# Kernel tuning notes

Hardware: AMD Instinct MI355X
Metric: run time of the kernel (lower is better)

Reference implementation:

```python
import jax, jax.numpy as jnp
import numpy as np

# DREAMPlace IDXST_IDCT (a.k.a. idsct2): y[u,v] = sum_p sum_q x[p,q] * sin(pi*p*(u+0.5)/M) * cos(pi*q*(v+0.5)/N)
# i.e. IDXST (inverse discrete sine transform, DST-III-like, unnormalized) along the M axis
# and IDCT (DCT-III-like, unnormalized, full weight on k=0) along the N axis.
# Computed with the classic 2N-padded FFT trick using the precomputed twiddles
# expk[k] = exp(-1j*pi*k/(2N)) stored as [N,2] (real, imag), matching precompute_expk.

def _idxt_spectrum(x, expk):
    """F[u] = sum_k x[k] * exp(-1j*pi*k*(2u+1)/(2N)), along last axis.
    Re(F) is the IDCT sum (cos), -Im(F) is the IDXST sum (sin)."""
    N = x.shape[-1]
    c = (x * expk[..., 0]) + 1j * (x * expk[..., 1])  # x[k] * exp(-j*pi*k/(2N))
    z = jnp.concatenate([c, jnp.zeros_like(c)], axis=-1)  # zero-pad to 2N
    return jnp.fft.fft(z, axis=-1)[..., :N]


def idct_1d(x, expk):
    # y[u] = sum_k x[k] cos(pi*k*(2u+1)/(2N))
    return _idxt_spectrum(x, expk).real


def idxst_1d(x, expk):
    # y[u] = sum_k x[k] sin(pi*k*(2u+1)/(2N))
    return -_idxt_spectrum(x, expk).imag


def _make_expk(L):
    k = jnp.arange(L, dtype=jnp.float32) * (np.pi / (2.0 * L))
    return jnp.stack([jnp.cos(k), -jnp.sin(k)], axis=-1)  # exp(-j*pi*k/(2L))


def setup_inputs() -> dict:
    M, N = 4096, 4096
    key = jax.random.key(0)
    x = jax.random.normal(key, (M, N), dtype=jnp.float32)
    return {"x": x, "expkM": _make_expk(M), "expkN": _make_expk(N)}


def reference(x, expkM, expkN):
    # IDCT along the last dim (N), then IDXST along the second-to-last dim (M):
    # idxst(idct(x)^T)^T
    t = idct_1d(x, expkN)                                        # [M, N]
    y = idxst_1d(t.swapaxes(-2, -1), expkM).swapaxes(-2, -1)     # [M, N]
    return y
```

## Files before the change

kernel.cpp:

```cpp
#include <hip/hip_runtime.h>
#include <hip/hip_bf16.h>
#include <stdint.h>
#include <cmath>


typedef __attribute__((ext_vector_type(4))) float f32x4;
typedef __attribute__((ext_vector_type(8))) unsigned short u16x8;
typedef __attribute__((ext_vector_type(8))) __bf16 bf16x8;

__device__ __forceinline__ unsigned short f2bf(float f) {
  union { float f; unsigned u; } v; v.f = f;
  unsigned u = v.u + 0x7fffu + ((v.u >> 16) & 1u);
  return (unsigned short)(u >> 16);
}
__device__ __forceinline__ float bf2f(unsigned short h) {
  union { unsigned u; float f; } v; v.u = ((unsigned)h) << 16;
  return v.f;
}

__global__ void convert_deint_kernel(const f32x4* __restrict__ x,
                                     u16x8* __restrict__ xe,
                                     u16x8* __restrict__ xo, int n16) {
  int idx = blockIdx.x * blockDim.x + threadIdx.x;
  if (idx >= n16) return;
  f32x4 a = x[4 * idx], b = x[4 * idx + 1], c = x[4 * idx + 2],
        d = x[4 * idx + 3];
  u16x8 e, o;
  e[0] = f2bf(a[0]); o[0] = f2bf(a[1]); e[1] = f2bf(a[2]); o[1] = f2bf(a[3]);
  e[2] = f2bf(b[0]); o[2] = f2bf(b[1]); e[3] = f2bf(b[2]); o[3] = f2bf(b[3]);
  e[4] = f2bf(c[0]); o[4] = f2bf(c[1]); e[5] = f2bf(c[2]); o[5] = f2bf(c[3]);
  e[6] = f2bf(d[0]); o[6] = f2bf(d[1]); e[7] = f2bf(d[2]); o[7] = f2bf(d[3]);
  xe[idx] = e; xo[idx] = o;
}

__global__ void gen_half_kernel(u16x8* __restrict__ Pe, u16x8* __restrict__ Po,
                                int isSin, int jshift, int jmask,
                                unsigned mask4L, float sc) {
  int idx = blockIdx.x * blockDim.x + threadIdx.x;
  int i = idx >> jshift;
  int jb = (idx & jmask) * 8;
  unsigned tp = 2u * (unsigned)i + 1u;
  unsigned re = (2u * (unsigned)jb * tp) & mask4L;
  unsigned ro = (re + tp) & mask4L;
  unsigned step = (2u * tp) & mask4L;
  u16x8 pe, po;
#pragma unroll
  for (int t = 0; t < 8; t++) {
    float se_, ce_, so_, co_;
    __sincosf((float)re * sc, &se_, &ce_);
    __sincosf((float)ro * sc, &so_, &co_);
    pe[t] = f2bf(isSin ? se_ : ce_);
    po[t] = f2bf(isSin ? so_ : co_);
    re = (re + step) & mask4L;
    ro = (ro + step) & mask4L;
  }
  Pe[idx] = pe;
  Po[idx] = po;
}

template <bool OUT_BF16>
__global__ __launch_bounds__(256, 2) void btgemm_kernel(
    const unsigned short* __restrict__ A0,
    const unsigned short* __restrict__ A1,
    const unsigned short* __restrict__ B0,
    const unsigned short* __restrict__ B1,
    void* __restrict__ C0v, void* __restrict__ C1v, int Ndim, int K) {
  __shared__ unsigned short As[128 * 32];
  __shared__ unsigned short Bs[128 * 32];

  const unsigned short* A = blockIdx.z ? A1 : A0;
  const unsigned short* Bt = blockIdx.z ? B1 : B0;
  void* C = blockIdx.z ? C1v : C0v;

  const int tid = threadIdx.x;
  const int m0 = blockIdx.y * 128;
  const int n0 = blockIdx.x * 128;

  const int wave = tid >> 6;
  const int lane = tid & 63;
  const int wm = (wave & 1) * 64;
  const int wn = (wave >> 1) * 64;
  const int l16 = lane & 15;
  const int quad = lane >> 4;

  f32x4 acc[4][4];
#pragma unroll
  for (int i = 0; i < 4; i++)
#pragma unroll
    for (int j = 0; j < 4; j++) acc[i][j] = f32x4{0.f, 0.f, 0.f, 0.f};

  const int rs0 = wave * 16 + (lane >> 2);
  const int rs1 = 64 + rs0;
  const int cs = (lane & 3) * 8;
  const unsigned short* Ag0 = A + (size_t)(m0 + rs0) * K + cs;
  const unsigned short* Ag1 = A + (size_t)(m0 + rs1) * K + cs;
  const unsigned short* Bg0 = Bt + (size_t)(n0 + rs0) * K + cs;
  const unsigned short* Bg1 = Bt + (size_t)(n0 + rs1) * K + cs;
  unsigned short* Al0 = As + wave * 512;
  unsigned short* Al1 = As + 2048 + wave * 512;
  unsigned short* Bl0 = Bs + wave * 512;
  unsigned short* Bl1 = Bs + 2048 + wave * 512;

  for (int k0 = 0; k0 < K; k0 += 32) {
    __builtin_amdgcn_global_load_lds(
        (const __attribute__((address_space(1))) void*)(Ag0 + k0),
        (__attribute__((address_space(3))) void*)Al0, 16, 0, 0);
    __builtin_amdgcn_global_load_lds(
        (const __attribute__((address_space(1))) void*)(Ag1 + k0),
        (__attribute__((address_space(3))) void*)Al1, 16, 0, 0);
    __builtin_amdgcn_global_load_lds(
        (const __attribute__((address_space(1))) void*)(Bg0 + k0),
        (__attribute__((address_space(3))) void*)Bl0, 16, 0, 0);
    __builtin_amdgcn_global_load_lds(
        (const __attribute__((address_space(1))) void*)(Bg1 + k0),
        (__attribute__((address_space(3))) void*)Bl1, 16, 0, 0);
    __syncthreads();

    bf16x8 af[4], bfr[4];
#pragma unroll
    for (int i = 0; i < 4; i++) {
      af[i]  = *(const bf16x8*)(As + (wm + i * 16 + l16) * 32 + quad * 8);
      bfr[i] = *(const bf16x8*)(Bs + (wn + i * 16 + l16) * 32 + quad * 8);
    }
#pragma unroll
    for (int i = 0; i < 4; i++)
#pragma unroll
      for (int j = 0; j < 4; j++)
        acc[i][j] = __builtin_amdgcn_mfma_f32_16x16x32_bf16(af[i], bfr[j],
                                                            acc[i][j], 0, 0, 0);
    __syncthreads();
  }

#pragma unroll
  for (int i = 0; i < 4; i++) {
#pragma unroll
    for (int j = 0; j < 4; j++) {
      int col = n0 + wn + j * 16 + l16;
      int rowb = m0 + wm + i * 16 + quad * 4;
#pragma unroll
      for (int r = 0; r < 4; r++) {
        float v = acc[i][j][r];
        if (OUT_BF16)
          ((unsigned short*)C)[(size_t)(rowb + r) * Ndim + col] = f2bf(v);
        else
          ((float*)C)[(size_t)(rowb + r) * Ndim + col] = v;
      }
    }
  }
}

__global__ void bfly1_kernel(const u16x8* __restrict__ E1,
                             const u16x8* __restrict__ O1,
                             u16x8* __restrict__ tTe, u16x8* __restrict__ tTo,
                             int pshift, int pmask, int Nrows, int Mh8) {
  int idx = blockIdx.x * blockDim.x + threadIdx.x;
  int v = idx >> pshift;
  int pu = idx & pmask;
  u16x8 e0 = E1[2 * idx], e1 = E1[2 * idx + 1];
  u16x8 o0 = O1[2 * idx], o1 = O1[2 * idx + 1];
  u16x8 tet, tot, teb, tob;
#pragma unroll
  for (int k = 0; k < 4; k++) {
    float ee = bf2f(e0[2 * k]), eo = bf2f(e0[2 * k + 1]);
    float oe = bf2f(o0[2 * k]), oo = bf2f(o0[2 * k + 1]);
    tet[k] = f2bf(ee + oe); tot[k] = f2bf(eo + oo);
    teb[k] = f2bf(ee - oe); tob[k] = f2bf(eo - oo);
  }
#pragma unroll
  for (int k = 0; k < 4; k++) {
    float ee = bf2f(e1[2 * k]), eo = bf2f(e1[2 * k + 1]);
    float oe = bf2f(o1[2 * k]), oo = bf2f(o1[2 * k + 1]);
    tet[4 + k] = f2bf(ee + oe); tot[4 + k] = f2bf(eo + oo);
    teb[4 + k] = f2bf(ee - oe); tob[4 + k] = f2bf(eo - oo);
  }
  tTe[idx] = tet;
  tTo[idx] = tot;
  int idxb = (Nrows - 1 - v) * Mh8 + pu;
  tTe[idxb] = teb;
  tTo[idxb] = tob;
}

__global__ void bfly2_kernel(const f32x4* __restrict__ E2,
                             const f32x4* __restrict__ O2,
                             f32x4* __restrict__ y, int vshift, int vmask,
                             int Mrows, int N4) {
  int idx = blockIdx.x * blockDim.x + threadIdx.x;
  int u = idx >> vshift;
  int vu = (idx & vmask) * 4;
  int baseb = (Mrows - 1 - u) * N4 + vu;
  int baset = u * N4 + vu;
#pragma unroll
  for (int t = 0; t < 4; t++) {
    f32x4 e = E2[4 * idx + t];
    f32x4 o = O2[4 * idx + t];
    y[baset + t] = e + o;
    y[baseb + t] = o - e;
  }
}

extern "C" void kernel_launch(void* const* d_in, const int* in_sizes, int n_in,
                              void* d_out, int out_size, void* d_ws,
                              size_t ws_size, hipStream_t stream) {
  const float* x = (const float*)d_in[0];
  const int M = in_sizes[1] / 2;
  const int N = in_sizes[2] / 2;
  const size_t MN = (size_t)M * N;

  unsigned short* ws = (unsigned short*)d_ws;
  unsigned short* xe = ws;
  unsigned short* xo = ws + MN / 2;
  unsigned short* Ae = ws + MN;
  unsigned short* Ao = ws + MN + MN / 4;
  unsigned short* E1 = ws + MN * 3 / 2;
  unsigned short* O1 = ws + MN * 2;
  unsigned short* tTe = ws + MN * 5 / 2;
  unsigned short* tTo = ws + MN * 3;
  float* E2 = (float*)ws;
  float* O2 = (float*)(ws + MN * 3 / 2);

  int shiftN = 0; while ((1 << shiftN) < N) shiftN++;
  int shiftM = 0; while ((1 << shiftM) < M) shiftM++;

  int n16 = (int)(MN / 16);
  convert_deint_kernel<<<(n16 + 255) / 256, 256, 0, stream>>>(
      (const f32x4*)x, (u16x8*)xe, (u16x8*)xo, n16);

  {
    int threads = (N / 2) * (N / 2) / 8;
    gen_half_kernel<<<threads / 256, 256, 0, stream>>>(
        (u16x8*)Ae, (u16x8*)Ao, 0, shiftN - 4, (N / 16) - 1,
        (unsigned)(4 * N - 1), (float)(3.14159265358979323846 / (2.0 * N)));
  }

  btgemm_kernel<true><<<dim3(M / 128, (N / 2) / 128, 2), 256, 0, stream>>>(
      Ae, Ao, xe, xo, E1, O1, M, N / 2);

  {
    int threads = (int)(MN / 32);
    bfly1_kernel<<<threads / 256, 256, 0, stream>>>(
        (const u16x8*)E1, (const u16x8*)O1, (u16x8*)tTe, (u16x8*)tTo,
        shiftM - 4, (M / 16) - 1, N, M / 16);
  }

  {
    int threads = (M / 2) * (M / 2) / 8;
    gen_half_kernel<<<threads / 256, 256, 0, stream>>>(
        (u16x8*)Ae, (u16x8*)Ao, 1, shiftM - 4, (M / 16) - 1,
        (unsigned)(4 * M - 1), (float)(3.14159265358979323846 / (2.0 * M)));
  }

  btgemm_kernel<false><<<dim3(N / 128, (M / 2) / 128, 2), 256, 0, stream>>>(
      Ae, Ao, tTe, tTo, E2, O2, N, M / 2);

  {
    int threads = (int)(MN / 32);
    bfly2_kernel<<<threads / 256, 256, 0, stream>>>(
        (const f32x4*)E2, (const f32x4*)O2, (f32x4*)d_out, shiftN - 4,
        (N / 16) - 1, M, N / 4);
  }
}
```

Measured before the change: 321.8 us.

## Fuse even/odd GEMMs and butterfly combine into a single GEMM epilogue

Each GEMM block now computes both the even and odd half-products one after the other, keeping two accumulator sets, and applies the butterfly (sum and difference with mirrored rows) directly in the epilogue. This removes the two standalone butterfly kernels and the round trip of the intermediate E/O buffers through global memory. In exchange the grid has half as many blocks, each doing twice the K work, and holds 32 accumulator vectors, which raises register pressure and may reduce occupancy. The epilogue stores are scattered: strided bf16 writes with an even/odd column split in stage 1 and mirrored fp32 rows in stage 2.

```diff
diff --git a/kernel.cpp b/kernel.cpp
--- a/kernel.cpp
+++ b/kernel.cpp
@@ -12,10 +12,6 @@
   union { float f; unsigned u; } v; v.f = f;
   unsigned u = v.u + 0x7fffu + ((v.u >> 16) & 1u);
   return (unsigned short)(u >> 16);
-}
-__device__ __forceinline__ float bf2f(unsigned short h) {
-  union { unsigned u; float f; } v; v.u = ((unsigned)h) << 16;
-  return v.f;
 }
 
 __global__ void convert_deint_kernel(const f32x4* __restrict__ x,
@@ -58,19 +54,16 @@
   Po[idx] = po;
 }
 
-template <bool OUT_BF16>
-__global__ __launch_bounds__(256, 2) void btgemm_kernel(
-    const unsigned short* __restrict__ A0,
-    const unsigned short* __restrict__ A1,
-    const unsigned short* __restrict__ B0,
-    const unsigned short* __restrict__ B1,
-    void* __restrict__ C0v, void* __restrict__ C1v, int Ndim, int K) {
+template <int STAGE>
+__global__ __launch_bounds__(256, 2) void btgemm_bfly_kernel(
+    const unsigned short* __restrict__ Ae,
+    const unsigned short* __restrict__ Ao,
+    const unsigned short* __restrict__ Be,
+    const unsigned short* __restrict__ Bo,
+    void* __restrict__ out0, void* __restrict__ out1,
+    int outStride, int K, int Lfull) {
   __shared__ unsigned short As[128 * 32];
   __shared__ unsigned short Bs[128 * 32];
-
-  const unsigned short* A = blockIdx.z ? A1 : A0;
-  const unsigned short* Bt = blockIdx.z ? B1 : B0;
-  void* C = blockIdx.z ? C1v : C0v;
 
   const int tid = threadIdx.x;
   const int m0 = blockIdx.y * 128;
@@ -83,118 +76,87 @@
   const int l16 = lane & 15;
   const int quad = lane >> 4;
 
-  f32x4 acc[4][4];
-#pragma unroll
-  for (int i = 0; i < 4; i++)
-#pragma unroll
-    for (int j = 0; j < 4; j++) acc[i][j] = f32x4{0.f, 0.f, 0.f, 0.f};
-
   const int rs0 = wave * 16 + (lane >> 2);
   const int rs1 = 64 + rs0;
   const int cs = (lane & 3) * 8;
-  const unsigned short* Ag0 = A + (size_t)(m0 + rs0) * K + cs;
-  const unsigned short* Ag1 = A + (size_t)(m0 + rs1) * K + cs;
-  const unsigned short* Bg0 = Bt + (size_t)(n0 + rs0) * K + cs;
-  const unsigned short* Bg1 = Bt + (size_t)(n0 + rs1) * K + cs;
   unsigned short* Al0 = As + wave * 512;
   unsigned short* Al1 = As + 2048 + wave * 512;
   unsigned short* Bl0 = Bs + wave * 512;
   unsigned short* Bl1 = Bs + 2048 + wave * 512;
 
-  for (int k0 = 0; k0 < K; k0 += 32) {
-    __builtin_amdgcn_global_load_lds(
-        (const __attribute__((address_space(1))) void*)(Ag0 + k0),
-        (__attribute__((address_space(3))) void*)Al0, 16, 0, 0);
-    __builtin_amdgcn_global_load_lds(
-        (const __attribute__((address_space(1))) void*)(Ag1 + k0),
-        (__attribute__((address_space(3))) void*)Al1, 16, 0, 0);
-    __builtin_amdgcn_global_load_lds(
-        (const __attribute__((address_space(1))) void*)(Bg0 + k0),
-        (__attribute__((address_space(3))) void*)Bl0, 16, 0, 0);
-    __builtin_amdgcn_global_load_lds(
-        (const __attribute__((address_space(1))) void*)(Bg1 + k0),
-        (__attribute__((address_space(3))) void*)Bl1, 16, 0, 0);
-    __syncthreads();
-
-    bf16x8 af[4], bfr[4];
-#pragma unroll
-    for (int i = 0; i < 4; i++) {
-      af[i]  = *(const bf16x8*)(As + (wm + i * 16 + l16) * 32 + quad * 8);
-      bfr[i] = *(const bf16x8*)(Bs + (wn + i * 16 + l16) * 32 + quad * 8);
+  f32x4 accE[4][4], accO[4][4];
+
+  auto kloop = [&](const unsigned short* __restrict__ A,
+                   const unsigned short* __restrict__ Bt,
+                   f32x4 (&acc)[4][4]) {
+#pragma unroll
+    for (int i = 0; i < 4; i++)
+#pragma unroll
+      for (int j = 0; j < 4; j++) acc[i][j] = f32x4{0.f, 0.f, 0.f, 0.f};
+
+    const unsigned short* Ag0 = A + (size_t)(m0 + rs0) * K + cs;
+    const unsigned short* Ag1 = A + (size_t)(m0 + rs1) * K + cs;
+    const unsigned short* Bg0 = Bt + (size_t)(n0 + rs0) * K + cs;
+    const unsigned short* Bg1 = Bt + (size_t)(n0 + rs1) * K + cs;
+
+    for (int k0 = 0; k0 < K; k0 += 32) {
+      __builtin_amdgcn_global_load_lds(
+          (const __attribute__((address_space(1))) void*)(Ag0 + k0),
+          (__attribute__((address_space(3))) void*)Al0, 16, 0, 0);
+      __builtin_amdgcn_global_load_lds(
+          (const __attribute__((address_space(1))) void*)(Ag1 + k0),
+          (__attribute__((address_space(3))) void*)Al1, 16, 0, 0);
+      __builtin_amdgcn_global_load_lds(
+          (const __attribute__((address_space(1))) void*)(Bg0 + k0),
+          (__attribute__((address_space(3))) void*)Bl0, 16, 0, 0);
+      __builtin_amdgcn_global_load_lds(
+          (const __attribute__((address_space(1))) void*)(Bg1 + k0),
+          (__attribute__((address_space(3))) void*)Bl1, 16, 0, 0);
+      __syncthreads();
+
+      bf16x8 af[4], bfr[4];
+#pragma unroll
+      for (int i = 0; i < 4; i++) {
+        af[i]  = *(const bf16x8*)(As + (wm + i * 16 + l16) * 32 + quad * 8);
+        bfr[i] = *(const bf16x8*)(Bs + (wn + i * 16 + l16) * 32 + quad * 8);
+      }
+#pragma unroll
+      for (int i = 0; i < 4; i++)
+#pragma unroll
+        for (int j = 0; j < 4; j++)
+          acc[i][j] = __builtin_amdgcn_mfma_f32_16x16x32_bf16(
+              af[i], bfr[j], acc[i][j], 0, 0, 0);
+      __syncthreads();
     }
-#pragma unroll
-    for (int i = 0; i < 4; i++)
-#pragma unroll
-      for (int j = 0; j < 4; j++)
-        acc[i][j] = __builtin_amdgcn_mfma_f32_16x16x32_bf16(af[i], bfr[j],
-                                                            acc[i][j], 0, 0, 0);
-    __syncthreads();
-  }
+  };
+
+  kloop(Ae, Be, accE);
+  kloop(Ao, Bo, accO);
 
 #pragma unroll
   for (int i = 0; i < 4; i++) {
 #pragma unroll
     for (int j = 0; j < 4; j++) {
-      int col = n0 + wn + j * 16 + l16;
-      int rowb = m0 + wm + i * 16 + quad * 4;
+      int n = n0 + wn + j * 16 + l16;
+      int mb = m0 + wm + i * 16 + quad * 4;
 #pragma unroll
       for (int r = 0; r < 4; r++) {
-        float v = acc[i][j][r];
-        if (OUT_BF16)
-          ((unsigned short*)C)[(size_t)(rowb + r) * Ndim + col] = f2bf(v);
-        else
-          ((float*)C)[(size_t)(rowb + r) * Ndim + col] = v;
+        float e = accE[i][j][r];
+        float o = accO[i][j][r];
+        int m = mb + r;
+        if (STAGE == 1) {
+          unsigned short* mat =
+              (n & 1) ? (unsigned short*)out1 : (unsigned short*)out0;
+          int col = n >> 1;
+          mat[(size_t)m * outStride + col] = f2bf(e + o);
+          mat[(size_t)(Lfull - 1 - m) * outStride + col] = f2bf(e - o);
+        } else {
+          float* y = (float*)out0;
+          y[(size_t)m * outStride + n] = e + o;
+          y[(size_t)(Lfull - 1 - m) * outStride + n] = o - e;
+        }
       }
     }
-  }
-}
-
-__global__ void bfly1_kernel(const u16x8* __restrict__ E1,
-                             const u16x8* __restrict__ O1,
-                             u16x8* __restrict__ tTe, u16x8* __restrict__ tTo,
-                             int pshift, int pmask, int Nrows, int Mh8) {
-  int idx = blockIdx.x * blockDim.x + threadIdx.x;
-  int v = idx >> pshift;
-  int pu = idx & pmask;
-  u16x8 e0 = E1[2 * idx], e1 = E1[2 * idx + 1];
-  u16x8 o0 = O1[2 * idx], o1 = O1[2 * idx + 1];
-  u16x8 tet, tot, teb, tob;
-#pragma unroll
-  for (int k = 0; k < 4; k++) {
-    float ee = bf2f(e0[2 * k]), eo = bf2f(e0[2 * k + 1]);
-    float oe = bf2f(o0[2 * k]), oo = bf2f(o0[2 * k + 1]);
-    tet[k] = f2bf(ee + oe); tot[k] = f2bf(eo + oo);
-    teb[k] = f2bf(ee - oe); tob[k] = f2bf(eo - oo);
-  }
-#pragma unroll
-  for (int k = 0; k < 4; k++) {
-    float ee = bf2f(e1[2 * k]), eo = bf2f(e1[2 * k + 1]);
-    float oe = bf2f(o1[2 * k]), oo = bf2f(o1[2 * k + 1]);
-    tet[4 + k] = f2bf(ee + oe); tot[4 + k] = f2bf(eo + oo);
-    teb[4 + k] = f2bf(ee - oe); tob[4 + k] = f2bf(eo - oo);
-  }
-  tTe[idx] = tet;
-  tTo[idx] = tot;
-  int idxb = (Nrows - 1 - v) * Mh8 + pu;
-  tTe[idxb] = teb;
-  tTo[idxb] = tob;
-}
-
-__global__ void bfly2_kernel(const f32x4* __restrict__ E2,
-                             const f32x4* __restrict__ O2,
-                             f32x4* __restrict__ y, int vshift, int vmask,
-                             int Mrows, int N4) {
-  int idx = blockIdx.x * blockDim.x + threadIdx.x;
-  int u = idx >> vshift;
-  int vu = (idx & vmask) * 4;
-  int baseb = (Mrows - 1 - u) * N4 + vu;
-  int baset = u * N4 + vu;
-#pragma unroll
-  for (int t = 0; t < 4; t++) {
-    f32x4 e = E2[4 * idx + t];
-    f32x4 o = O2[4 * idx + t];
-    y[baset + t] = e + o;
-    y[baseb + t] = o - e;
   }
 }
 
@@ -211,12 +173,8 @@
   unsigned short* xo = ws + MN / 2;
   unsigned short* Ae = ws + MN;
   unsigned short* Ao = ws + MN + MN / 4;
-  unsigned short* E1 = ws + MN * 3 / 2;
-  unsigned short* O1 = ws + MN * 2;
-  unsigned short* tTe = ws + MN * 5 / 2;
-  unsigned short* tTo = ws + MN * 3;
-  float* E2 = (float*)ws;
-  float* O2 = (float*)(ws + MN * 3 / 2);
+  unsigned short* tTe = ws + MN * 3 / 2;
+  unsigned short* tTo = ws + MN * 2;
 
   int shiftN = 0; while ((1 << shiftN) < N) shiftN++;
   int shiftM = 0; while ((1 << shiftM) < M) shiftM++;
@@ -232,15 +190,8 @@
         (unsigned)(4 * N - 1), (float)(3.14159265358979323846 / (2.0 * N)));
   }
 
-  btgemm_kernel<true><<<dim3(M / 128, (N / 2) / 128, 2), 256, 0, stream>>>(
-      Ae, Ao, xe, xo, E1, O1, M, N / 2);
-
-  {
-    int threads = (int)(MN / 32);
-    bfly1_kernel<<<threads / 256, 256, 0, stream>>>(
-        (const u16x8*)E1, (const u16x8*)O1, (u16x8*)tTe, (u16x8*)tTo,
-        shiftM - 4, (M / 16) - 1, N, M / 16);
-  }
+  btgemm_bfly_kernel<1><<<dim3(M / 128, (N / 2) / 128), 256, 0, stream>>>(
+      Ae, Ao, xe, xo, tTe, tTo, M / 2, N / 2, N);
 
   {
     int threads = (M / 2) * (M / 2) / 8;
@@ -249,13 +200,6 @@
         (unsigned)(4 * M - 1), (float)(3.14159265358979323846 / (2.0 * M)));
   }
 
-  btgemm_kernel<false><<<dim3(N / 128, (M / 2) / 128, 2), 256, 0, stream>>>(
-      Ae, Ao, tTe, tTo, E2, O2, N, M / 2);
-
-  {
-    int threads = (int)(MN / 32);
-    bfly2_kernel<<<threads / 256, 256, 0, stream>>>(
-        (const f32x4*)E2, (const f32x4*)O2, (f32x4*)d_out, shiftN - 4,
-        (N / 16) - 1, M, N / 4);
-  }
-}
+  btgemm_bfly_kernel<2><<<dim3(N / 128, (M / 2) / 128), 256, 0, stream>>>(
+      Ae, Ao, tTe, tTo, d_out, nullptr, N, M / 2, M);
+}
```

Result: no change. 323.7 us (+0.6%).
